# Kernel tuning notes

Measured on AMD Instinct MI355X. Metric: run time of the kernel, lower is better.

## Reference

```python
import jax, jax.numpy as jnp
import numpy as np

B, T, DM, DS = 8, 2048, 1024, 256
BASE_DECAY = 0.05


def _lin(k, out_dim, in_dim):
    return jax.random.normal(k, (out_dim, in_dim), jnp.float32) / np.sqrt(in_dim).astype(np.float32)


def setup_inputs() -> dict:
    key = jax.random.key(0)
    ks = jax.random.split(key, 18)
    return {
        "x": jax.random.normal(ks[0], (B, T, DM), jnp.float32),
        "prev_state": jax.random.normal(ks[1], (B, DS), jnp.float32),
        "W_in": _lin(ks[2], DS, DM),
        "W_x": _lin(ks[3], DS, DM),
        "W_s": _lin(ks[4], DS, DS),
        "W_out": _lin(ks[5], DM, DS),
        "W_gx": _lin(ks[6], DS, DM),
        "b_gx": jax.random.normal(ks[7], (DS,), jnp.float32) * 0.02,
        "W_gs": _lin(ks[8], DS, DS),
        "b_gs": jax.random.normal(ks[9], (DS,), jnp.float32) * 0.02,
        "W_dc": _lin(ks[10], DS, DM + DS),
        "b_dc": jax.random.normal(ks[11], (DS,), jnp.float32) * 0.02,
        "W_pp": _lin(ks[12], DS, 2 * DS),
        "b_pp": jax.random.normal(ks[13], (DS,), jnp.float32) * 0.02,
        "W_pg": _lin(ks[14], DS, DS),
        "b_pg": jax.random.normal(ks[15], (DS,), jnp.float32) * 0.02,
    }


def reference(x, prev_state, W_in, W_x, W_s, W_out, W_gx, b_gx, W_gs, b_gs,
              W_dc, b_dc, W_pp, b_pp, W_pg, b_pg):
    # torch Linear: y = x @ W.T (+ b); W is [out, in]
    lin = lambda v, W: jnp.einsum('bti,oi->bto', v, W)
    Bx, Tx, _ = x.shape
    delta = lin(x, W_in)                                   # [B,T,DS]
    s_prev = jnp.broadcast_to(prev_state[:, None, :], (Bx, Tx, prev_state.shape[-1]))
    ctx = jnp.concatenate([x, s_prev], axis=-1)            # [B,T,DM+DS]
    decay = jnp.exp(-BASE_DECAY * jnp.clip(jax.nn.sigmoid(lin(ctx, W_dc) + b_dc), 0.0, 1.0))
    s_pred = s_prev * decay + delta + lin(x, W_x) + 0.5 * lin(s_prev, W_s)
    perturb_in = jnp.concatenate([s_pred, s_prev], axis=-1)  # [B,T,2*DS]
    perturb_vec = jnp.tanh(lin(perturb_in, W_pp) + b_pp)
    perturb_strength = jax.nn.sigmoid(lin(s_prev, W_pg) + b_pg)
    s_corrected = s_pred + perturb_strength * perturb_vec
    gate_in = jax.nn.sigmoid(lin(x, W_gx) + b_gx)
    gate_state = jax.nn.sigmoid(lin(s_prev, W_gs) + b_gs)
    h = s_corrected * gate_in * gate_state
    out = lin(h, W_out)                                    # [B,T,DM]
    return out, h[:, -1, :]
```

## Files before the change

kernel.cpp:

```cpp
#include <hip/hip_runtime.h>
#include <hip/hip_bf16.h>
#include <math.h>


typedef __attribute__((ext_vector_type(4)))  float f32x4;
typedef __attribute__((ext_vector_type(8)))  short bf16x8;

#define DEV static __device__ __forceinline__

DEV float bf2f(short u) {
  union { float f; unsigned i; } v; v.i = ((unsigned)(unsigned short)u) << 16; return v.f;
}
DEV short f2bf(float f) {
  union { float f; unsigned i; } v; v.f = f;
  unsigned x = v.i;
  return (short)((x + 0x7fffu + ((x >> 16) & 1u)) >> 16);
}
DEV unsigned pk_bf16(float lo, float hi) {
  __hip_bfloat162 h = __float22bfloat162_rn(make_float2(lo, hi));
  return *(unsigned*)&h;
}
DEV float sigmoidf_(float x) { return 1.f / (1.f + expf(-x)); }

DEV void gl16(const void* g, void* l) {
  __builtin_amdgcn_global_load_lds(
      (const __attribute__((address_space(1))) void*)(g),
      (__attribute__((address_space(3))) void*)(l), 16, 0, 0);
}

DEV void stage_tile(const short* gA, const short* gB, short* As, short* Bs,
                    int lda, int ldb, int w, int lane) {
  const int rsub = lane >> 2, kc = (lane & 3) * 8;
#pragma unroll
  for (int j = 0; j < 2; ++j) {
    const int seg = w * 2 + j;
    const int r = seg * 16 + rsub;
    gl16(gA + (size_t)r * lda + kc, As + seg * 512);
    gl16(gB + (size_t)r * ldb + kc, Bs + seg * 512);
  }
}

DEV void kstep(const short* Asb, const short* Bsb, int wr, int wc, int arow, int ag,
               f32x4 (&acc)[4][4]) {
  bf16x8 af[4], bfv[4];
#pragma unroll
  for (int mi = 0; mi < 4; ++mi)
    af[mi] = *(const bf16x8*)(Asb + (wr * 64 + mi * 16 + arow) * 32 + ag * 8);
#pragma unroll
  for (int ni = 0; ni < 4; ++ni)
    bfv[ni] = *(const bf16x8*)(Bsb + (wc * 64 + ni * 16 + arow) * 32 + ag * 8);
#pragma unroll
  for (int mi = 0; mi < 4; ++mi)
#pragma unroll
    for (int ni = 0; ni < 4; ++ni)
      acc[mi][ni] = __builtin_amdgcn_mfma_f32_16x16x32_bf16(af[mi], bfv[ni], acc[mi][ni], 0, 0, 0);
}

static const size_t OFF_S    = 0;
static const size_t OFF_G    = 8388608;
static const size_t OFF_XBF  = 25165824;
static const size_t OFF_WCAT = OFF_XBF + 33554432;
static const size_t OFF_WPP  = OFF_WCAT + 1572864;
static const size_t OFF_WOUT = OFF_WPP + 131072;
static const size_t OFF_VEC  = OFF_WOUT + 524288;

__global__ __launch_bounds__(256, 1) void cvt_x_k(const float* __restrict__ x,
                                                  short* __restrict__ xbf) {
  const size_t i = ((size_t)blockIdx.x * 256 + threadIdx.x) * 8;
  const float4 a = *(const float4*)(x + i);
  const float4 b = *(const float4*)(x + i + 4);
  uint4 o;
  o.x = pk_bf16(a.x, a.y); o.y = pk_bf16(a.z, a.w);
  o.z = pk_bf16(b.x, b.y); o.w = pk_bf16(b.z, b.w);
  *(uint4*)(xbf + i) = o;
}

__global__ __launch_bounds__(256, 1) void prep_w_k(const float* __restrict__ W_in,
                                                   const float* __restrict__ W_x,
                                                   const float* __restrict__ W_gx,
                                                   const float* __restrict__ W_dc,
                                                   const float* __restrict__ W_pp,
                                                   const float* __restrict__ W_out,
                                                   short* __restrict__ wcat,
                                                   short* __restrict__ wpp,
                                                   short* __restrict__ wout) {
  const int idx = (int)blockIdx.x * 256 + (int)threadIdx.x;
  const int N_WCAT = 768 * 1024, N_WPP = 256 * 256;
  if (idx < N_WCAT) {
    const int r = idx >> 10, k = idx & 1023;
    const int g = r / 192, j = r % 192;
    float v;
    if (j < 64)       v = W_in[(g * 64 + j) * 1024 + k] + W_x[(g * 64 + j) * 1024 + k];
    else if (j < 128) v = W_gx[(g * 64 + j - 64) * 1024 + k];
    else              v = W_dc[(g * 64 + j - 128) * 1280 + k];
    wcat[idx] = f2bf(v);
  } else if (idx < N_WCAT + N_WPP) {
    const int j = idx - N_WCAT, o = j >> 8, k = j & 255;
    wpp[j] = f2bf(W_pp[o * 512 + k]);
  } else {
    const int j = idx - N_WCAT - N_WPP, o = j >> 8, k = j & 255;
    wout[j] = f2bf(W_out[o * 256 + k]);
  }
}

__global__ __launch_bounds__(256, 1) void state_k(const float* __restrict__ prev,
                                                  const float* __restrict__ Ws,
                                                  const float* __restrict__ Wdc,
                                                  const float* __restrict__ bdc,
                                                  const float* __restrict__ Wpp,
                                                  const float* __restrict__ bpp,
                                                  const float* __restrict__ Wpg,
                                                  const float* __restrict__ bpg,
                                                  const float* __restrict__ Wgs,
                                                  const float* __restrict__ bgs,
                                                  float* __restrict__ vecs) {
  const int bid = (int)blockIdx.x;
  const int b = bid / 20, rem = bid % 20, m = rem >> 2, oq = rem & 3;
  const int tid = (int)threadIdx.x, lane = tid & 63, w = tid >> 6;
  const float4 sv = *(const float4*)(prev + b * 256 + lane * 4);
  const float* Wb; const float* bias; int stride, off;
  if (m == 0)      { Wb = Wdc; stride = 1280; off = 1024; bias = bdc; }
  else if (m == 1) { Wb = Ws;  stride = 256;  off = 0;    bias = nullptr; }
  else if (m == 2) { Wb = Wpp; stride = 512;  off = 256;  bias = bpp; }
  else if (m == 3) { Wb = Wpg; stride = 256;  off = 0;    bias = bpg; }
  else             { Wb = Wgs; stride = 256;  off = 0;    bias = bgs; }
  const int o0 = oq * 64 + w * 16;
#pragma unroll 4
  for (int i = 0; i < 16; ++i) {
    const int o = o0 + i;
    const float4 wv = *(const float4*)(Wb + (size_t)o * stride + off + lane * 4);
    float p = wv.x * sv.x + wv.y * sv.y + wv.z * sv.z + wv.w * sv.w;
#pragma unroll
    for (int d = 32; d >= 1; d >>= 1) p += __shfl_xor(p, d, 64);
    if (lane == 0) {
      float r = (m == 1) ? 0.5f * p : p + bias[o];
      if (m >= 3) r = sigmoidf_(r);
      vecs[m * 2048 + b * 256 + o] = r;
    }
  }
}

__global__ __launch_bounds__(256) void gemm1sg_k(const short* __restrict__ A,
                                                 const short* __restrict__ Bm,
                                                 const float* __restrict__ prev,
                                                 const float* __restrict__ bgx,
                                                 const float* __restrict__ vecs,
                                                 short* __restrict__ S,
                                                 short* __restrict__ G) {
  __shared__ short As[2][4096];
  __shared__ short Bs[2][6144];
  const int tid = (int)threadIdx.x, lane = tid & 63, w = tid >> 6;
  int bid = (int)blockIdx.x;
  bid = (bid & 7) * 64 + (bid >> 3);
  const int mt = bid >> 2, nt = bid & 3;
  const int m0 = mt * 128, b = m0 >> 11;
  const short* gA = A + (size_t)m0 * 1024;
  const short* gB = Bm + (size_t)(nt * 192) * 1024;
  const int rsub = lane >> 2, kc = (lane & 3) * 8;

  f32x4 acc[2][12];
#pragma unroll
  for (int mi = 0; mi < 2; ++mi)
#pragma unroll
    for (int ni = 0; ni < 12; ++ni)
#pragma unroll
      for (int r = 0; r < 4; ++r) acc[mi][ni][r] = 0.f;

#define STAGE1(buf, t)                                                        \
  {                                                                           \
    _Pragma("unroll")                                                         \
    for (int j = 0; j < 2; ++j) {                                             \
      const int seg = w * 2 + j;                                              \
      gl16(gA + (size_t)(seg * 16 + rsub) * 1024 + (t) * 32 + kc,             \
           As[buf] + seg * 512);                                              \
    }                                                                         \
    _Pragma("unroll")                                                         \
    for (int i = 0; i < 3; ++i) {                                             \
      const int Gr = i * 256 + w * 64 + lane;                                 \
      gl16(gB + (size_t)(Gr >> 2) * 1024 + (t) * 32 + ((Gr & 3) * 8),         \
           Bs[buf] + (i * 256 + w * 64) * 8);                                 \
    }                                                                         \
  }

  STAGE1(0, 0);
  __syncthreads();
  const int arow = lane & 15, ag = lane >> 4;
#pragma unroll 1
  for (int t = 0; t < 32; ++t) {
    if (t < 31) STAGE1((t + 1) & 1, t + 1);
    const short* Asb = As[t & 1];
    const short* Bsb = Bs[t & 1];
    bf16x8 af[2];
#pragma unroll
    for (int mi = 0; mi < 2; ++mi)
      af[mi] = *(const bf16x8*)(Asb + (w * 32 + mi * 16 + arow) * 32 + ag * 8);
#pragma unroll
    for (int ni = 0; ni < 12; ++ni) {
      const bf16x8 bf = *(const bf16x8*)(Bsb + (ni * 16 + arow) * 32 + ag * 8);
#pragma unroll
      for (int mi = 0; mi < 2; ++mi)
        acc[mi][ni] = __builtin_amdgcn_mfma_f32_16x16x32_bf16(af[mi], bf, acc[mi][ni], 0, 0, 0);
    }
    __syncthreads();
  }
#undef STAGE1

  const int quad = lane >> 4;
#pragma unroll
  for (int cidx = 0; cidx < 4; ++cidx) {
    const int cg = nt * 64 + cidx * 16 + arow;
    const float sdc = vecs[0 * 2048 + b * 256 + cg];
    const float sws = vecs[1 * 2048 + b * 256 + cg];
    const float pv  = prev[b * 256 + cg];
    const float bg  = bgx[cg];
#pragma unroll
    for (int mi = 0; mi < 2; ++mi)
#pragma unroll
      for (int r = 0; r < 4; ++r) {
        const int row = m0 + w * 32 + mi * 16 + quad * 4 + r;
        const float dec = expf(-0.05f * sigmoidf_(acc[mi][8 + cidx][r] + sdc));
        const float sp = pv * dec + acc[mi][cidx][r] + sws;
        const float g = sigmoidf_(acc[mi][4 + cidx][r] + bg);
        S[(size_t)row * 256 + cg] = f2bf(sp);
        G[(size_t)row * 256 + cg] = f2bf(g);
      }
  }
}

__global__ __launch_bounds__(256) void gemm2h_k(const short* __restrict__ S,
                                                const short* __restrict__ G,
                                                const short* __restrict__ Wpp,
                                                const float* __restrict__ vecs,
                                                short* __restrict__ H,
                                                float* __restrict__ out) {
  __shared__ short As[2][4096];
  __shared__ short Bs[2][4096];
  const int tid = (int)threadIdx.x, lane = tid & 63, w = tid >> 6;
  const int wr = w >> 1, wc = w & 1;
  int bid = (int)blockIdx.x;
  bid = (bid & 7) * 32 + (bid >> 3);
  const int m0 = (bid >> 1) * 128, n0 = (bid & 1) * 128;
  const int b = m0 >> 11;
  const short* gA = S + (size_t)m0 * 256;
  const short* gB = Wpp + (size_t)n0 * 256;

  f32x4 acc[4][4];
#pragma unroll
  for (int mi = 0; mi < 4; ++mi)
#pragma unroll
    for (int ni = 0; ni < 4; ++ni)
#pragma unroll
      for (int r = 0; r < 4; ++r) acc[mi][ni][r] = 0.f;

  stage_tile(gA, gB, As[0], Bs[0], 256, 256, w, lane);
  __syncthreads();
  const int arow = lane & 15, ag = lane >> 4;
#pragma unroll 1
  for (int t = 0; t < 8; ++t) {
    if (t < 7)
      stage_tile(gA + (t + 1) * 32, gB + (t + 1) * 32,
                 As[(t + 1) & 1], Bs[(t + 1) & 1], 256, 256, w, lane);
    kstep(As[t & 1], Bs[t & 1], wr, wc, arow, ag, acc);
    __syncthreads();
  }
#pragma unroll
  for (int mi = 0; mi < 4; ++mi)
#pragma unroll
    for (int ni = 0; ni < 4; ++ni) {
      const int col = n0 + wc * 64 + ni * 16 + (lane & 15);
      const float spp  = vecs[2 * 2048 + b * 256 + col];
      const float pstr = vecs[3 * 2048 + b * 256 + col];
      const float gst  = vecs[4 * 2048 + b * 256 + col];
#pragma unroll
      for (int r = 0; r < 4; ++r) {
        const int row = m0 + wr * 64 + mi * 16 + (lane >> 4) * 4 + r;
        const float pv = tanhf(acc[mi][ni][r] + spp);
        const float sp = bf2f(S[(size_t)row * 256 + col]);
        const float h = (sp + pstr * pv) * bf2f(G[(size_t)row * 256 + col]) * gst;
        H[(size_t)row * 256 + col] = f2bf(h);
        if ((row & 2047) == 2047) out[16777216 + b * 256 + col] = h;
      }
    }
}

__global__ __launch_bounds__(256) void gemm3_k(const short* __restrict__ H,
                                               const short* __restrict__ Wout,
                                               float* __restrict__ out) {
  __shared__ short As[2][4096];
  __shared__ short Bs[2][4096];
  const int tid = (int)threadIdx.x, lane = tid & 63, w = tid >> 6;
  const int wr = w >> 1, wc = w & 1;
  int bid = (int)blockIdx.x;
  bid = (bid & 7) * 128 + (bid >> 3);
  const int m0 = (bid >> 3) * 128, n0 = (bid & 7) * 128;
  const short* gA = H + (size_t)m0 * 256;
  const short* gB = Wout + (size_t)n0 * 256;

  f32x4 acc[4][4];
#pragma unroll
  for (int mi = 0; mi < 4; ++mi)
#pragma unroll
    for (int ni = 0; ni < 4; ++ni)
#pragma unroll
      for (int r = 0; r < 4; ++r) acc[mi][ni][r] = 0.f;

  stage_tile(gA, gB, As[0], Bs[0], 256, 256, w, lane);
  __syncthreads();
  const int arow = lane & 15, ag = lane >> 4;
#pragma unroll 1
  for (int t = 0; t < 8; ++t) {
    if (t < 7)
      stage_tile(gA + (t + 1) * 32, gB + (t + 1) * 32,
                 As[(t + 1) & 1], Bs[(t + 1) & 1], 256, 256, w, lane);
    kstep(As[t & 1], Bs[t & 1], wr, wc, arow, ag, acc);
    __syncthreads();
  }
#pragma unroll
  for (int mi = 0; mi < 4; ++mi)
#pragma unroll
    for (int ni = 0; ni < 4; ++ni) {
      const int col = n0 + wc * 64 + ni * 16 + (lane & 15);
#pragma unroll
      for (int r = 0; r < 4; ++r) {
        const int row = m0 + wr * 64 + mi * 16 + (lane >> 4) * 4 + r;
        out[(size_t)row * 1024 + col] = acc[mi][ni][r];
      }
    }
}

extern "C" void kernel_launch(void* const* d_in, const int* in_sizes, int n_in,
                              void* d_out, int out_size, void* d_ws, size_t ws_size,
                              hipStream_t stream) {
  (void)in_sizes; (void)n_in; (void)out_size; (void)ws_size;
  const float* x      = (const float*)d_in[0];
  const float* prev   = (const float*)d_in[1];
  const float* W_in   = (const float*)d_in[2];
  const float* W_x    = (const float*)d_in[3];
  const float* W_s    = (const float*)d_in[4];
  const float* W_out  = (const float*)d_in[5];
  const float* W_gx   = (const float*)d_in[6];
  const float* b_gx   = (const float*)d_in[7];
  const float* W_gs   = (const float*)d_in[8];
  const float* b_gs   = (const float*)d_in[9];
  const float* W_dc   = (const float*)d_in[10];
  const float* b_dc   = (const float*)d_in[11];
  const float* W_pp   = (const float*)d_in[12];
  const float* b_pp   = (const float*)d_in[13];
  const float* W_pg   = (const float*)d_in[14];
  const float* b_pg   = (const float*)d_in[15];

  char* ws = (char*)d_ws;
  short* S    = (short*)(ws + OFF_S);
  short* G    = (short*)(ws + OFF_G);
  short* xbf  = (short*)(ws + OFF_XBF);
  short* H    = (short*)(ws + OFF_XBF);
  short* wcat = (short*)(ws + OFF_WCAT);
  short* wpp  = (short*)(ws + OFF_WPP);
  short* wout = (short*)(ws + OFF_WOUT);
  float* vecs = (float*)(ws + OFF_VEC);
  float* out  = (float*)d_out;

  cvt_x_k<<<8192, 256, 0, stream>>>(x, xbf);
  prep_w_k<<<4352, 256, 0, stream>>>(W_in, W_x, W_gx, W_dc, W_pp, W_out, wcat, wpp, wout);
  state_k<<<160, 256, 0, stream>>>(prev, W_s, W_dc, b_dc, W_pp, b_pp, W_pg, b_pg, W_gs, b_gs, vecs);
  gemm1sg_k<<<512, 256, 0, stream>>>(xbf, wcat, prev, b_gx, vecs, S, G);
  gemm2h_k<<<256, 256, 0, stream>>>(S, G, wpp, vecs, H, out);
  gemm3_k<<<1024, 256, 0, stream>>>(H, wout, out);
}
```

Before: 115.4 us.

## Merge prep kernels into one launch and halve GEMM1 N-tile for more blocks

Three preprocessing kernels (x conversion, weight packing, state-vector matvecs) become one kernel that dispatches on block index, removing two launches and their gaps. GEMM1 now uses 96-column N tiles (32 columns per output group) instead of 192, doubling the grid to 1024 blocks. The weight interleaving in the packing step changes to match. Smaller tiles raise occupancy and parallelism on the GPU but reload the A tile twice as often.

```diff
diff --git a/kernel.cpp b/kernel.cpp
--- a/kernel.cpp
+++ b/kernel.cpp
@@ -64,78 +64,68 @@
 static const size_t OFF_WOUT = OFF_WPP + 131072;
 static const size_t OFF_VEC  = OFF_WOUT + 524288;
 
-__global__ __launch_bounds__(256, 1) void cvt_x_k(const float* __restrict__ x,
-                                                  short* __restrict__ xbf) {
-  const size_t i = ((size_t)blockIdx.x * 256 + threadIdx.x) * 8;
-  const float4 a = *(const float4*)(x + i);
-  const float4 b = *(const float4*)(x + i + 4);
-  uint4 o;
-  o.x = pk_bf16(a.x, a.y); o.y = pk_bf16(a.z, a.w);
-  o.z = pk_bf16(b.x, b.y); o.w = pk_bf16(b.z, b.w);
-  *(uint4*)(xbf + i) = o;
-}
-
-__global__ __launch_bounds__(256, 1) void prep_w_k(const float* __restrict__ W_in,
-                                                   const float* __restrict__ W_x,
-                                                   const float* __restrict__ W_gx,
-                                                   const float* __restrict__ W_dc,
-                                                   const float* __restrict__ W_pp,
-                                                   const float* __restrict__ W_out,
-                                                   short* __restrict__ wcat,
-                                                   short* __restrict__ wpp,
-                                                   short* __restrict__ wout) {
-  const int idx = (int)blockIdx.x * 256 + (int)threadIdx.x;
-  const int N_WCAT = 768 * 1024, N_WPP = 256 * 256;
-  if (idx < N_WCAT) {
-    const int r = idx >> 10, k = idx & 1023;
-    const int g = r / 192, j = r % 192;
-    float v;
-    if (j < 64)       v = W_in[(g * 64 + j) * 1024 + k] + W_x[(g * 64 + j) * 1024 + k];
-    else if (j < 128) v = W_gx[(g * 64 + j - 64) * 1024 + k];
-    else              v = W_dc[(g * 64 + j - 128) * 1280 + k];
-    wcat[idx] = f2bf(v);
-  } else if (idx < N_WCAT + N_WPP) {
-    const int j = idx - N_WCAT, o = j >> 8, k = j & 255;
-    wpp[j] = f2bf(W_pp[o * 512 + k]);
+__global__ __launch_bounds__(256, 1) void prep_all_k(
+    const float* __restrict__ x, short* __restrict__ xbf,
+    const float* __restrict__ W_in, const float* __restrict__ W_x,
+    const float* __restrict__ W_gx, const float* __restrict__ W_dc,
+    const float* __restrict__ W_pp, const float* __restrict__ W_out,
+    short* __restrict__ wcat, short* __restrict__ wpp, short* __restrict__ wout,
+    const float* __restrict__ prev, const float* __restrict__ Ws,
+    const float* __restrict__ bdc, const float* __restrict__ bpp,
+    const float* __restrict__ Wpg, const float* __restrict__ bpg,
+    const float* __restrict__ Wgs, const float* __restrict__ bgs,
+    float* __restrict__ vecs) {
+  const int bid = (int)blockIdx.x, tid = (int)threadIdx.x;
+  if (bid < 8192) {
+    const size_t i = ((size_t)bid * 256 + tid) * 8;
+    const float4 a = *(const float4*)(x + i);
+    const float4 b = *(const float4*)(x + i + 4);
+    uint4 o;
+    o.x = pk_bf16(a.x, a.y); o.y = pk_bf16(a.z, a.w);
+    o.z = pk_bf16(b.x, b.y); o.w = pk_bf16(b.z, b.w);
+    *(uint4*)(xbf + i) = o;
+  } else if (bid < 12544) {
+    const int idx = (bid - 8192) * 256 + tid;
+    const int N_WCAT = 768 * 1024, N_WPP = 256 * 256;
+    if (idx < N_WCAT) {
+      const int r = idx >> 10, k = idx & 1023;
+      const int g = r / 96, j = r % 96;
+      float v;
+      if (j < 32)      v = W_in[(g * 32 + j) * 1024 + k] + W_x[(g * 32 + j) * 1024 + k];
+      else if (j < 64) v = W_gx[(g * 32 + j - 32) * 1024 + k];
+      else             v = W_dc[(g * 32 + j - 64) * 1280 + k];
+      wcat[idx] = f2bf(v);
+    } else if (idx < N_WCAT + N_WPP) {
+      const int j = idx - N_WCAT, o = j >> 8, k = j & 255;
+      wpp[j] = f2bf(W_pp[o * 512 + k]);
+    } else {
+      const int j = idx - N_WCAT - N_WPP, o = j >> 8, k = j & 255;
+      wout[j] = f2bf(W_out[o * 256 + k]);
+    }
   } else {
-    const int j = idx - N_WCAT - N_WPP, o = j >> 8, k = j & 255;
-    wout[j] = f2bf(W_out[o * 256 + k]);
-  }
-}
-
-__global__ __launch_bounds__(256, 1) void state_k(const float* __restrict__ prev,
-                                                  const float* __restrict__ Ws,
-                                                  const float* __restrict__ Wdc,
-                                                  const float* __restrict__ bdc,
-                                                  const float* __restrict__ Wpp,
-                                                  const float* __restrict__ bpp,
-                                                  const float* __restrict__ Wpg,
-                                                  const float* __restrict__ bpg,
-                                                  const float* __restrict__ Wgs,
-                                                  const float* __restrict__ bgs,
-                                                  float* __restrict__ vecs) {
-  const int bid = (int)blockIdx.x;
-  const int b = bid / 20, rem = bid % 20, m = rem >> 2, oq = rem & 3;
-  const int tid = (int)threadIdx.x, lane = tid & 63, w = tid >> 6;
-  const float4 sv = *(const float4*)(prev + b * 256 + lane * 4);
-  const float* Wb; const float* bias; int stride, off;
-  if (m == 0)      { Wb = Wdc; stride = 1280; off = 1024; bias = bdc; }
-  else if (m == 1) { Wb = Ws;  stride = 256;  off = 0;    bias = nullptr; }
-  else if (m == 2) { Wb = Wpp; stride = 512;  off = 256;  bias = bpp; }
-  else if (m == 3) { Wb = Wpg; stride = 256;  off = 0;    bias = bpg; }
-  else             { Wb = Wgs; stride = 256;  off = 0;    bias = bgs; }
-  const int o0 = oq * 64 + w * 16;
+    const int sb = bid - 12544;
+    const int b = sb / 20, rem = sb % 20, m = rem >> 2, oq = rem & 3;
+    const int lane = tid & 63, w = tid >> 6;
+    const float4 sv = *(const float4*)(prev + b * 256 + lane * 4);
+    const float* Wb; const float* bias; int stride, off;
+    if (m == 0)      { Wb = W_dc; stride = 1280; off = 1024; bias = bdc; }
+    else if (m == 1) { Wb = Ws;   stride = 256;  off = 0;    bias = nullptr; }
+    else if (m == 2) { Wb = W_pp; stride = 512;  off = 256;  bias = bpp; }
+    else if (m == 3) { Wb = Wpg;  stride = 256;  off = 0;    bias = bpg; }
+    else             { Wb = Wgs;  stride = 256;  off = 0;    bias = bgs; }
+    const int o0 = oq * 64 + w * 16;
 #pragma unroll 4
-  for (int i = 0; i < 16; ++i) {
-    const int o = o0 + i;
-    const float4 wv = *(const float4*)(Wb + (size_t)o * stride + off + lane * 4);
-    float p = wv.x * sv.x + wv.y * sv.y + wv.z * sv.z + wv.w * sv.w;
-#pragma unroll
-    for (int d = 32; d >= 1; d >>= 1) p += __shfl_xor(p, d, 64);
-    if (lane == 0) {
-      float r = (m == 1) ? 0.5f * p : p + bias[o];
-      if (m >= 3) r = sigmoidf_(r);
-      vecs[m * 2048 + b * 256 + o] = r;
+    for (int i = 0; i < 16; ++i) {
+      const int o = o0 + i;
+      const float4 wv = *(const float4*)(Wb + (size_t)o * stride + off + lane * 4);
+      float p = wv.x * sv.x + wv.y * sv.y + wv.z * sv.z + wv.w * sv.w;
+#pragma unroll
+      for (int d = 32; d >= 1; d >>= 1) p += __shfl_xor(p, d, 64);
+      if (lane == 0) {
+        float r = (m == 1) ? 0.5f * p : p + bias[o];
+        if (m >= 3) r = sigmoidf_(r);
+        vecs[m * 2048 + b * 256 + o] = r;
+      }
     }
   }
 }
@@ -148,21 +138,21 @@
                                                  short* __restrict__ S,
                                                  short* __restrict__ G) {
   __shared__ short As[2][4096];
-  __shared__ short Bs[2][6144];
+  __shared__ short Bs[2][3072];
   const int tid = (int)threadIdx.x, lane = tid & 63, w = tid >> 6;
   int bid = (int)blockIdx.x;
-  bid = (bid & 7) * 64 + (bid >> 3);
-  const int mt = bid >> 2, nt = bid & 3;
+  bid = (bid & 7) * 128 + (bid >> 3);
+  const int mt = bid >> 3, ntg = bid & 7;
   const int m0 = mt * 128, b = m0 >> 11;
   const short* gA = A + (size_t)m0 * 1024;
-  const short* gB = Bm + (size_t)(nt * 192) * 1024;
+  const short* gB = Bm + (size_t)(ntg * 96) * 1024;
   const int rsub = lane >> 2, kc = (lane & 3) * 8;
 
-  f32x4 acc[2][12];
+  f32x4 acc[2][6];
 #pragma unroll
   for (int mi = 0; mi < 2; ++mi)
 #pragma unroll
-    for (int ni = 0; ni < 12; ++ni)
+    for (int ni = 0; ni < 6; ++ni)
 #pragma unroll
       for (int r = 0; r < 4; ++r) acc[mi][ni][r] = 0.f;
 
@@ -174,11 +164,15 @@
       gl16(gA + (size_t)(seg * 16 + rsub) * 1024 + (t) * 32 + kc,             \
            As[buf] + seg * 512);                                              \
     }                                                                         \
-    _Pragma("unroll")                                                         \
-    for (int i = 0; i < 3; ++i) {                                             \
-      const int Gr = i * 256 + w * 64 + lane;                                 \
+    {                                                                         \
+      const int Gr = w * 64 + lane;                                           \
       gl16(gB + (size_t)(Gr >> 2) * 1024 + (t) * 32 + ((Gr & 3) * 8),         \
-           Bs[buf] + (i * 256 + w * 64) * 8);                                 \
+           Bs[buf] + w * 512);                                                \
+    }                                                                         \
+    if (w < 2) {                                                              \
+      const int Gr = 256 + w * 64 + lane;                                     \
+      gl16(gB + (size_t)(Gr >> 2) * 1024 + (t) * 32 + ((Gr & 3) * 8),         \
+           Bs[buf] + 2048 + w * 512);                                         \
     }                                                                         \
   }
 
@@ -195,7 +189,7 @@
     for (int mi = 0; mi < 2; ++mi)
       af[mi] = *(const bf16x8*)(Asb + (w * 32 + mi * 16 + arow) * 32 + ag * 8);
 #pragma unroll
-    for (int ni = 0; ni < 12; ++ni) {
+    for (int ni = 0; ni < 6; ++ni) {
       const bf16x8 bf = *(const bf16x8*)(Bsb + (ni * 16 + arow) * 32 + ag * 8);
 #pragma unroll
       for (int mi = 0; mi < 2; ++mi)
@@ -207,8 +201,8 @@
 
   const int quad = lane >> 4;
 #pragma unroll
-  for (int cidx = 0; cidx < 4; ++cidx) {
-    const int cg = nt * 64 + cidx * 16 + arow;
+  for (int nj = 0; nj < 2; ++nj) {
+    const int cg = ntg * 32 + nj * 16 + arow;
     const float sdc = vecs[0 * 2048 + b * 256 + cg];
     const float sws = vecs[1 * 2048 + b * 256 + cg];
     const float pv  = prev[b * 256 + cg];
@@ -218,9 +212,9 @@
 #pragma unroll
       for (int r = 0; r < 4; ++r) {
         const int row = m0 + w * 32 + mi * 16 + quad * 4 + r;
-        const float dec = expf(-0.05f * sigmoidf_(acc[mi][8 + cidx][r] + sdc));
-        const float sp = pv * dec + acc[mi][cidx][r] + sws;
-        const float g = sigmoidf_(acc[mi][4 + cidx][r] + bg);
+        const float dec = expf(-0.05f * sigmoidf_(acc[mi][4 + nj][r] + sdc));
+        const float sp = pv * dec + acc[mi][nj][r] + sws;
+        const float g = sigmoidf_(acc[mi][2 + nj][r] + bg);
         S[(size_t)row * 256 + cg] = f2bf(sp);
         G[(size_t)row * 256 + cg] = f2bf(g);
       }
@@ -360,10 +354,10 @@
   float* vecs = (float*)(ws + OFF_VEC);
   float* out  = (float*)d_out;
 
-  cvt_x_k<<<8192, 256, 0, stream>>>(x, xbf);
-  prep_w_k<<<4352, 256, 0, stream>>>(W_in, W_x, W_gx, W_dc, W_pp, W_out, wcat, wpp, wout);
-  state_k<<<160, 256, 0, stream>>>(prev, W_s, W_dc, b_dc, W_pp, b_pp, W_pg, b_pg, W_gs, b_gs, vecs);
-  gemm1sg_k<<<512, 256, 0, stream>>>(xbf, wcat, prev, b_gx, vecs, S, G);
+  prep_all_k<<<12704, 256, 0, stream>>>(x, xbf, W_in, W_x, W_gx, W_dc, W_pp, W_out,
+                                        wcat, wpp, wout, prev, W_s, b_dc, b_pp,
+                                        W_pg, b_pg, W_gs, b_gs, vecs);
+  gemm1sg_k<<<1024, 256, 0, stream>>>(xbf, wcat, prev, b_gx, vecs, S, G);
   gemm2h_k<<<256, 256, 0, stream>>>(S, G, wpp, vecs, H, out);
   gemm3_k<<<1024, 256, 0, stream>>>(H, wout, out);
 }
```

After: 109.5 us. 1.05x faster.
